# Kernel tuning notes

Hardware: AMD Instinct MI355X
Metric: run time of the kernel (lower is better)

## Reference

```python
import jax, jax.numpy as jnp
import numpy as np

EPS = 1e-5

def setup_inputs() -> dict:
    key = jax.random.key(0)
    ks = jax.random.split(key, 6)
    n, m, k, c_in, c_out = 200000, 50000, 16, 128, 256
    p = jax.random.normal(ks[0], (n, 3), dtype=jnp.float32)
    x = jax.random.normal(ks[1], (n, c_in), dtype=jnp.float32)
    o = jnp.sort(jax.random.randint(ks[2], (4,), 0, n)).astype(jnp.int64)
    n_p = jax.random.normal(ks[3], (m, 3), dtype=jnp.float32)
    knn_idx = jax.random.randint(ks[4], (m, k), 0, n).astype(jnp.int64)
    n_o = jnp.sort(jax.random.randint(ks[5], (4,), 0, m)).astype(jnp.int64)
    norm_w = jnp.ones((c_in,), dtype=jnp.float32)
    norm_b = jnp.zeros((c_in,), dtype=jnp.float32)
    W = jax.random.normal(jax.random.fold_in(key, 7), (c_out, c_in), dtype=jnp.float32) * (1.0 / np.sqrt(c_in))
    return {"p": p, "x": x, "o": o, "n_p": n_p, "knn_idx": knn_idx, "n_o": n_o,
            "norm_w": norm_w, "norm_b": norm_b, "W": W}

def reference(p, x, o, n_p, knn_idx, n_o, norm_w, norm_b, W):
    # Gather neighbor features: [m, k, c_in] (use_xyz=False so grouped_xyz is unused)
    feats = x[knn_idx]
    # LayerNorm over channel dim
    mu = jnp.mean(feats, axis=-1, keepdims=True)
    var = jnp.mean(jnp.square(feats - mu), axis=-1, keepdims=True)
    h = (feats - mu) * jax.lax.rsqrt(var + EPS) * norm_w + norm_b
    # Linear (no bias): torch Linear y = h @ W.T, W: [c_out, c_in]
    y = jnp.einsum('mkc,oc->mko', h, W)
    # MaxPool1d over the k neighbors
    out = jnp.max(y, axis=1)  # [m, c_out]
    return (out, n_p, n_o)
```

## Files before the change

### kernel.cpp

```cpp
#include <hip/hip_runtime.h>


#define C_IN   128
#define C_OUT  256
#define KNN    16
#define LN_EPS 1e-5f
#define BQ     4
#define ROWS   (BQ * KNN)
#define WAVES  8
#define BLOCK  (WAVES * 64)
#define NBLK   1024
#define BROW   128
#define BUFB   (ROWS * BROW)
#define BSCL   16.0f
#define IBSCL  (1.0f / 16.0f)

typedef __attribute__((ext_vector_type(8))) short  short8;
typedef __attribute__((ext_vector_type(4))) short  short4_t;
typedef __attribute__((ext_vector_type(8))) __bf16 bf16x8;
typedef __attribute__((ext_vector_type(4))) float  f32x4;

__device__ __forceinline__ short f2bf_bits(float f) {
    unsigned u = __float_as_uint(f);
    u += 0x7fffu + ((u >> 16) & 1u);
    return (short)(u >> 16);
}

#if defined(__has_builtin) && __has_builtin(__builtin_amdgcn_cvt_pk_fp8_f32)
__device__ __forceinline__ unsigned pk2fp8(float a, float b, unsigned old, bool hi) {
    return hi ? (unsigned)__builtin_amdgcn_cvt_pk_fp8_f32(a, b, (int)old, true)
              : (unsigned)__builtin_amdgcn_cvt_pk_fp8_f32(a, b, (int)old, false);
}
#else
__device__ __forceinline__ unsigned fp8e4m3_byte(float f) {
    unsigned u = __float_as_uint(f);
    const unsigned sgn = (u >> 24) & 0x80u;
    const float af = __uint_as_float(u & 0x7fffffffu);
    if (!(af < 448.f)) return sgn | 0x7Eu;
    if (af < 0.015625f) {
        int q = (int)(af * 512.f + 0.5f);
        return (q > 7) ? (sgn | 0x08u) : (sgn | (unsigned)q);
    }
    unsigned au = u & 0x7fffffffu;
    au += 0x7FFFFu + ((au >> 20) & 1u);
    const int e = (int)(au >> 23) - 127;
    if (e > 8) return sgn | 0x7Eu;
    return sgn | ((unsigned)(e + 7) << 3) | ((au >> 20) & 7u);
}
__device__ __forceinline__ unsigned pk2fp8(float a, float b, unsigned old, bool hi) {
    const unsigned p = fp8e4m3_byte(a) | (fp8e4m3_byte(b) << 8);
    return hi ? ((old & 0xffffu) | (p << 16)) : ((old & 0xffff0000u) | p);
}
#endif

__device__ __forceinline__ void gl_lds16b(const void* src, void* dst) {
    __builtin_amdgcn_global_load_lds(
        (const __attribute__((address_space(1))) void*)src,
        (__attribute__((address_space(3))) void*)dst, 16, 0, 0);
}

__global__ __launch_bounds__(256) void lnq_kernel(
    const float* __restrict__ x, unsigned* __restrict__ xq, int n)
{
    const int r = blockIdx.x * 8 + (threadIdx.x >> 5);
    const int c = threadIdx.x & 31;
    if (r >= n) return;
    const float4 v = *(const float4*)(x + (long long)r * C_IN + c * 4);
    float s1 = v.x + v.y + v.z + v.w;
    float s2 = v.x * v.x + v.y * v.y + v.z * v.z + v.w * v.w;
    #pragma unroll
    for (int off = 1; off < 32; off <<= 1) {
        s1 += __shfl_xor(s1, off);
        s2 += __shfl_xor(s2, off);
    }
    const float mu   = s1 * (1.f / 128.f);
    const float rstd = rsqrtf(s2 * (1.f / 128.f) - mu * mu + LN_EPS);
    unsigned p = pk2fp8((v.x - mu) * rstd, (v.y - mu) * rstd, 0u, false);
    p = pk2fp8((v.z - mu) * rstd, (v.w - mu) * rstd, p, true);
    xq[(long long)r * 32 + c] = p;
}

__global__ __launch_bounds__(BLOCK) void fused_gather_kernel(
    const unsigned char* __restrict__ xq, const int* __restrict__ knn,
    const float* __restrict__ nw, const float* __restrict__ nb,
    const float* __restrict__ W,
    const float* __restrict__ n_p, const int* __restrict__ n_o,
    float* __restrict__ out, float* __restrict__ out_np, float* __restrict__ out_no,
    int mq, int npcnt)
{
    __shared__ __align__(16) char Ash[2 * BUFB];

    const int tid  = threadIdx.x;
    const int lane = tid & 63;
    const int wave = tid >> 6;
    const int m16  = lane & 15;
    const int qd   = lane >> 4;

    const int g    = gridDim.x;
    const int nbat = (mq + BQ - 1) / BQ;
    const int nk   = mq * KNN;

    const int myrow = wave * 8 + (lane >> 3);
    const int sboff = ((lane & 7) ^ (myrow & 7)) * 16;

    int bat = blockIdx.x;
    int i0 = knn[min(bat * ROWS + myrow, nk - 1)];

    long  bfr[2][4];
    float cp0 = 0.f, cp1 = 0.f;
    #pragma unroll
    for (int s = 0; s < 4; ++s) {
        const int k0 = s * 32 + qd * 8;
        const float4 a0 = *(const float4*)(nw + k0);
        const float4 a1 = *(const float4*)(nw + k0 + 4);
        const float4 c0 = *(const float4*)(nb + k0);
        const float4 c1 = *(const float4*)(nb + k0 + 4);
        const float nwv[8] = {a0.x,a0.y,a0.z,a0.w,a1.x,a1.y,a1.z,a1.w};
        const float nbv[8] = {c0.x,c0.y,c0.z,c0.w,c1.x,c1.y,c1.z,c1.w};
        #pragma unroll
        for (int t = 0; t < 2; ++t) {
            const int n_ = wave * 32 + t * 16 + m16;
            const float4* wp = (const float4*)(W + n_ * C_IN + k0);
            const float4 w0 = wp[0], w1 = wp[1];
            const float wvv[8] = {w0.x,w0.y,w0.z,w0.w,w1.x,w1.y,w1.z,w1.w};
            float cacc = 0.f;
            #pragma unroll
            for (int j = 0; j < 8; ++j) cacc += nbv[j] * wvv[j];
            unsigned lo = pk2fp8(wvv[0]*nwv[0]*BSCL, wvv[1]*nwv[1]*BSCL, 0u, false);
            lo = pk2fp8(wvv[2]*nwv[2]*BSCL, wvv[3]*nwv[3]*BSCL, lo, true);
            unsigned hi = pk2fp8(wvv[4]*nwv[4]*BSCL, wvv[5]*nwv[5]*BSCL, 0u, false);
            hi = pk2fp8(wvv[6]*nwv[6]*BSCL, wvv[7]*nwv[7]*BSCL, hi, true);
            bfr[t][s] = (long)(((unsigned long long)hi << 32) | lo);
            if (t == 0) cp0 += cacc; else cp1 += cacc;
        }
    }
    cp0 += __shfl_xor(cp0, 16); cp0 += __shfl_xor(cp0, 32);
    cp1 += __shfl_xor(cp1, 16); cp1 += __shfl_xor(cp1, 32);

    gl_lds16b(xq + (long long)i0 * BROW + sboff, Ash + wave * 1024);
    const int b1 = (bat + g < nbat) ? (bat + g) : bat;
    int inext = knn[min(b1 * ROWS + myrow, nk - 1)];

    int buf = 0;
    for (; bat < nbat; bat += g) {
        __syncthreads();

        if (bat + g < nbat) {
            gl_lds16b(xq + (long long)inext * BROW + sboff,
                      Ash + (buf ^ 1) * BUFB + wave * 1024);
            const int b2 = (bat + 2 * g < nbat) ? (bat + 2 * g) : (bat + g);
            inext = knn[min(b2 * ROWS + myrow, nk - 1)];
        }

        #pragma unroll
        for (int jp = 0; jp < 2; ++jp) {
            float ra0, ra1, rb0, rb1;
            #pragma unroll
            for (int half = 0; half < 2; ++half) {
                const int ql = jp * 2 + half;
                const int r  = ql * 16 + m16;
                long afr[4];
                #pragma unroll
                for (int s = 0; s < 4; ++s) {
                    const int pos = (s * 2 + (qd >> 1)) ^ (r & 7);
                    afr[s] = *(const long*)&Ash[buf * BUFB + r * BROW + pos * 16 + (qd & 1) * 8];
                }
                f32x4 acc0 = {0,0,0,0}, acc1 = {0,0,0,0};
                #pragma unroll
                for (int s = 0; s < 4; ++s) {
                    acc0 = __builtin_amdgcn_mfma_f32_16x16x32_fp8_fp8(
                        afr[s], bfr[0][s], acc0, 0, 0, 0);
                    acc1 = __builtin_amdgcn_mfma_f32_16x16x32_fp8_fp8(
                        afr[s], bfr[1][s], acc1, 0, 0, 0);
                }
                float v0 = fmaxf(fmaxf(acc0[0], acc0[1]), fmaxf(acc0[2], acc0[3]));
                v0 = fmaxf(v0, __shfl_xor(v0, 16));
                v0 = fmaxf(v0, __shfl_xor(v0, 32));
                float v1 = fmaxf(fmaxf(acc1[0], acc1[1]), fmaxf(acc1[2], acc1[3]));
                v1 = fmaxf(v1, __shfl_xor(v1, 16));
                v1 = fmaxf(v1, __shfl_xor(v1, 32));
                if (half == 0) { ra0 = v0; ra1 = v1; }
                else           { rb0 = v0; rb1 = v1; }
            }
            const float s0 = (qd >> 1) ? rb0 : ra0;
            const float s1 = (qd >> 1) ? rb1 : ra1;
            const float val = ((qd & 1) ? s1 : s0) * IBSCL + ((qd & 1) ? cp1 : cp0);
            const int q = bat * BQ + jp * 2 + (qd >> 1);
            if (q < mq)
                out[q * C_OUT + wave * 32 + (qd & 1) * 16 + m16] = val;
        }
        buf ^= 1;
    }

    const int gtid = blockIdx.x * BLOCK + tid;
    const int gstr = g * BLOCK;
    const int np4 = npcnt >> 2;
    for (int i = gtid; i < np4; i += gstr)
        ((float4*)out_np)[i] = ((const float4*)n_p)[i];
    for (int i = (np4 << 2) + gtid; i < npcnt; i += gstr) out_np[i] = n_p[i];
    if (gtid < 4) out_no[gtid] = (float)n_o[gtid];
}

__global__ __launch_bounds__(256) void fused_inline_kernel(
    const float* __restrict__ x, const int* __restrict__ knn,
    const float* __restrict__ nw, const float* __restrict__ nb,
    const float* __restrict__ W,
    const float* __restrict__ n_p, const int* __restrict__ n_o,
    float* __restrict__ out, float* __restrict__ out_np, float* __restrict__ out_no,
    int mq, int npcnt)
{
    __shared__ __align__(16) short Ash[2 * 32 * C_IN];

    const int tid  = threadIdx.x;
    const int lane = tid & 63;
    const int wave = tid >> 6;
    const int m16  = lane & 15;
    const int qd   = lane >> 4;

    short8 bfrag[4][4];
    float  cpart[4] = {0.f, 0.f, 0.f, 0.f};
    #pragma unroll
    for (int s = 0; s < 4; ++s) {
        const int k0 = s * 32 + qd * 8;
        const float4 a0 = *(const float4*)(nw + k0);
        const float4 a1 = *(const float4*)(nw + k0 + 4);
        const float4 c0 = *(const float4*)(nb + k0);
        const float4 c1 = *(const float4*)(nb + k0 + 4);
        const float nwv[8] = {a0.x,a0.y,a0.z,a0.w,a1.x,a1.y,a1.z,a1.w};
        const float nbv[8] = {c0.x,c0.y,c0.z,c0.w,c1.x,c1.y,c1.z,c1.w};
        #pragma unroll
        for (int t = 0; t < 4; ++t) {
            const int n = wave * 64 + t * 16 + m16;
            const float4* wp = (const float4*)(W + n * C_IN + k0);
            const float4 w0 = wp[0], w1 = wp[1];
            const float wvv[8] = {w0.x,w0.y,w0.z,w0.w,w1.x,w1.y,w1.z,w1.w};
            short8 b;
            #pragma unroll
            for (int j = 0; j < 8; ++j) {
                b[j] = f2bf_bits(wvv[j] * nwv[j]);
                cpart[t] += nbv[j] * wvv[j];
            }
            bfrag[t][s] = b;
        }
    }
    #pragma unroll
    for (int t = 0; t < 4; ++t) {
        cpart[t] += __shfl_xor(cpart[t], 16);
        cpart[t] += __shfl_xor(cpart[t], 32);
    }
    const float cbias = (qd == 0) ? cpart[0] : (qd == 1) ? cpart[1]
                      : (qd == 2) ? cpart[2] : cpart[3];

    const int sr = tid >> 3;
    const int sc = tid & 7;

    const int nbat = (mq + 1) / 2;
    const int g = gridDim.x;
    const int nk = mq * KNN;

    int bat = blockIdx.x;
    float4 pf[4];
    int idxn;
    {
        const int id0 = knn[min(bat * 32 + sr, nk - 1)];
        const float* xr = x + (long long)id0 * C_IN + sc * 4;
        #pragma unroll
        for (int t = 0; t < 4; ++t) pf[t] = *(const float4*)(xr + t * 32);
        const int b1 = (bat + g < nbat) ? (bat + g) : bat;
        idxn = knn[min(b1 * 32 + sr, nk - 1)];
    }

    int buf = 0;
    for (; bat < nbat; bat += g) {
        float s1 = 0.f, s2 = 0.f;
        #pragma unroll
        for (int t = 0; t < 4; ++t) {
            s1 += pf[t].x + pf[t].y + pf[t].z + pf[t].w;
            s2 += pf[t].x*pf[t].x + pf[t].y*pf[t].y + pf[t].z*pf[t].z + pf[t].w*pf[t].w;
        }
        #pragma unroll
        for (int off = 1; off < 8; off <<= 1) {
            s1 += __shfl_xor(s1, off);
            s2 += __shfl_xor(s2, off);
        }
        const float mu   = s1 * (1.f / 128.f);
        const float rstd = rsqrtf(s2 * (1.f / 128.f) - mu * mu + LN_EPS);
        #pragma unroll
        for (int t = 0; t < 4; ++t) {
            short4_t hb;
            hb[0] = f2bf_bits((pf[t].x - mu) * rstd);
            hb[1] = f2bf_bits((pf[t].y - mu) * rstd);
            hb[2] = f2bf_bits((pf[t].z - mu) * rstd);
            hb[3] = f2bf_bits((pf[t].w - mu) * rstd);
            const int pb = ((sc >> 1) + 4 * t) ^ (sr & 15);
            *(short4_t*)&Ash[buf * 4096 + sr * 128 + pb * 8 + (sc & 1) * 4] = hb;
        }
        __syncthreads();

        if (bat + g < nbat) {
            const float* xr = x + (long long)idxn * C_IN + sc * 4;
            #pragma unroll
            for (int t = 0; t < 4; ++t) pf[t] = *(const float4*)(xr + t * 32);
            const int b2 = (bat + 2 * g < nbat) ? (bat + 2 * g) : (bat + g);
            idxn = knn[min(b2 * 32 + sr, nk - 1)];
        }

        #pragma unroll
        for (int ql = 0; ql < 2; ++ql) {
            short8 afrag[4];
            #pragma unroll
            for (int s = 0; s < 4; ++s) {
                const int pb = (s * 4 + qd) ^ m16;
                afrag[s] = *(const short8*)&Ash[buf * 4096 + (ql * 16 + m16) * 128 + pb * 8];
            }
            f32x4 acc[4] = {{0,0,0,0},{0,0,0,0},{0,0,0,0},{0,0,0,0}};
            #pragma unroll
            for (int s = 0; s < 4; ++s) {
                const bf16x8 av = __builtin_bit_cast(bf16x8, afrag[s]);
                #pragma unroll
                for (int t = 0; t < 4; ++t)
                    acc[t] = __builtin_amdgcn_mfma_f32_16x16x32_bf16(
                        av, __builtin_bit_cast(bf16x8, bfrag[t][s]), acc[t], 0, 0, 0);
            }
            float r[4];
            #pragma unroll
            for (int t = 0; t < 4; ++t) {
                float v = fmaxf(fmaxf(acc[t][0], acc[t][1]), fmaxf(acc[t][2], acc[t][3]));
                v = fmaxf(v, __shfl_xor(v, 16));
                v = fmaxf(v, __shfl_xor(v, 32));
                r[t] = v;
            }
            const float vout = ((qd == 0) ? r[0] : (qd == 1) ? r[1]
                              : (qd == 2) ? r[2] : r[3]) + cbias;
            const int q = bat * 2 + ql;
            if (q < mq) out[q * C_OUT + wave * 64 + lane] = vout;
        }
        buf ^= 1;
    }

    const int gtid = blockIdx.x * 256 + tid;
    const int gstr = g * 256;
    const int np4 = npcnt >> 2;
    for (int i = gtid; i < np4; i += gstr)
        ((float4*)out_np)[i] = ((const float4*)n_p)[i];
    for (int i = (np4 << 2) + gtid; i < npcnt; i += gstr) out_np[i] = n_p[i];
    if (gtid < 4) out_no[gtid] = (float)n_o[gtid];
}

extern "C" void kernel_launch(void* const* d_in, const int* in_sizes, int n_in,
                              void* d_out, int out_size, void* d_ws, size_t ws_size,
                              hipStream_t stream)
{
    const float* x   = (const float*)d_in[1];
    const float* n_p = (const float*)d_in[3];
    const int*   knn = (const int*)  d_in[4];
    const int*   n_o = (const int*)  d_in[5];
    const float* nw  = (const float*)d_in[6];
    const float* nb  = (const float*)d_in[7];
    const float* W   = (const float*)d_in[8];
    float* out = (float*)d_out;

    const int n     = in_sizes[1] / C_IN;
    const int mq    = in_sizes[4] / KNN;
    const int npcnt = in_sizes[3];
    float* out_np = out + (size_t)mq * C_OUT;
    float* out_no = out_np + npcnt;

    const size_t ws_need = (size_t)n * BROW;
    if (ws_size >= ws_need) {
        unsigned* xq = (unsigned*)d_ws;
        hipLaunchKernelGGL(lnq_kernel, dim3((n + 7) / 8), dim3(256), 0, stream,
                           x, xq, n);
        hipLaunchKernelGGL(fused_gather_kernel, dim3(NBLK), dim3(BLOCK), 0, stream,
                           (const unsigned char*)xq, knn, nw, nb, W, n_p, n_o,
                           out, out_np, out_no, mq, npcnt);
    } else {
        hipLaunchKernelGGL(fused_inline_kernel, dim3(NBLK), dim3(256), 0, stream,
                           x, knn, nw, nb, W, n_p, n_o, out, out_np, out_no, mq, npcnt);
    }
}
```

Baseline: 236.6 us.

## Deepen gather pipeline to four LDS buffers with preloaded neighbor indices

New measurement: 241.5 us. 1.02x slower.

```diff
diff --git a/kernel.cpp b/kernel.cpp
--- a/kernel.cpp
+++ b/kernel.cpp
@@ -12,6 +12,7 @@
 #define NBLK   1024
 #define BROW   128
 #define BUFB   (ROWS * BROW)
+#define NSLOT  16
 #define BSCL   16.0f
 #define IBSCL  (1.0f / 16.0f)
 
@@ -88,7 +89,8 @@
     float* __restrict__ out, float* __restrict__ out_np, float* __restrict__ out_no,
     int mq, int npcnt)
 {
-    __shared__ __align__(16) char Ash[2 * BUFB];
+    __shared__ __align__(16) char Ash[4 * BUFB];
+    __shared__ int idx_lds[NSLOT * ROWS];
 
     const int tid  = threadIdx.x;
     const int lane = tid & 63;
@@ -102,9 +104,13 @@
 
     const int myrow = wave * 8 + (lane >> 3);
     const int sboff = ((lane & 7) ^ (myrow & 7)) * 16;
-
-    int bat = blockIdx.x;
-    int i0 = knn[min(bat * ROWS + myrow, nk - 1)];
+    char* const dwave = Ash + wave * 1024;
+
+    for (int j = tid; j < NSLOT * ROWS; j += BLOCK) {
+        const long long bb = (long long)blockIdx.x + (long long)(j >> 6) * g;
+        const int bidx = (bb < nbat) ? (int)bb : (nbat - 1);
+        idx_lds[j] = knn[min(bidx * ROWS + (j & 63), nk - 1)];
+    }
 
     long  bfr[2][4];
     float cp0 = 0.f, cp1 = 0.f;
@@ -137,20 +143,31 @@
     cp0 += __shfl_xor(cp0, 16); cp0 += __shfl_xor(cp0, 32);
     cp1 += __shfl_xor(cp1, 16); cp1 += __shfl_xor(cp1, 32);
 
-    gl_lds16b(xq + (long long)i0 * BROW + sboff, Ash + wave * 1024);
-    const int b1 = (bat + g < nbat) ? (bat + g) : bat;
-    int inext = knn[min(b1 * ROWS + myrow, nk - 1)];
-
-    int buf = 0;
-    for (; bat < nbat; bat += g) {
-        __syncthreads();
-
-        if (bat + g < nbat) {
-            gl_lds16b(xq + (long long)inext * BROW + sboff,
-                      Ash + (buf ^ 1) * BUFB + wave * 1024);
-            const int b2 = (bat + 2 * g < nbat) ? (bat + 2 * g) : (bat + g);
-            inext = knn[min(b2 * ROWS + myrow, nk - 1)];
-        }
+    __syncthreads();
+
+    {
+        const int i0 = idx_lds[0 * ROWS + myrow];
+        const int i1 = idx_lds[1 * ROWS + myrow];
+        const int i2 = idx_lds[2 * ROWS + myrow];
+        gl_lds16b(xq + (((long long)i0) << 7) + sboff, dwave + 0 * BUFB);
+        gl_lds16b(xq + (((long long)i1) << 7) + sboff, dwave + 1 * BUFB);
+        gl_lds16b(xq + (((long long)i2) << 7) + sboff, dwave + 2 * BUFB);
+    }
+    int nextidx = idx_lds[3 * ROWS + myrow];
+    asm volatile("s_waitcnt vmcnt(2)" ::: "memory");
+    __builtin_amdgcn_s_barrier();
+    __builtin_amdgcn_sched_barrier(0);
+
+    const int L = (nbat - 1 - blockIdx.x) / g + 1;
+    for (int t = 0; t < L; ++t) {
+        const int bat = blockIdx.x + t * g;
+
+        gl_lds16b(xq + (((long long)nextidx) << 7) + sboff,
+                  dwave + ((t + 3) & 3) * BUFB);
+        const int ns = (t + 4 < NSLOT) ? (t + 4) : (NSLOT - 1);
+        nextidx = idx_lds[ns * ROWS + myrow];
+
+        const char* Ab = Ash + (t & 3) * BUFB;
 
         #pragma unroll
         for (int jp = 0; jp < 2; ++jp) {
@@ -163,7 +180,7 @@
                 #pragma unroll
                 for (int s = 0; s < 4; ++s) {
                     const int pos = (s * 2 + (qd >> 1)) ^ (r & 7);
-                    afr[s] = *(const long*)&Ash[buf * BUFB + r * BROW + pos * 16 + (qd & 1) * 8];
+                    afr[s] = *(const long*)(Ab + r * BROW + pos * 16 + (qd & 1) * 8);
                 }
                 f32x4 acc0 = {0,0,0,0}, acc1 = {0,0,0,0};
                 #pragma unroll
@@ -189,7 +206,10 @@
             if (q < mq)
                 out[q * C_OUT + wave * 32 + (qd & 1) * 16 + m16] = val;
         }
-        buf ^= 1;
+
+        asm volatile("s_waitcnt vmcnt(4)" ::: "memory");
+        __builtin_amdgcn_s_barrier();
+        __builtin_amdgcn_sched_barrier(0);
     }
 
     const int gtid = blockIdx.x * BLOCK + tid;
@@ -369,9 +389,12 @@
     const size_t ws_need = (size_t)n * BROW;
     if (ws_size >= ws_need) {
         unsigned* xq = (unsigned*)d_ws;
+        const int nbat = (mq + BQ - 1) / BQ;
+        int grid = (nbat < NBLK) ? nbat : NBLK;
+        while ((nbat + grid - 1) / grid + 3 > NSLOT) grid *= 2;
         hipLaunchKernelGGL(lnq_kernel, dim3((n + 7) / 8), dim3(256), 0, stream,
                            x, xq, n);
-        hipLaunchKernelGGL(fused_gather_kernel, dim3(NBLK), dim3(BLOCK), 0, stream,
+        hipLaunchKernelGGL(fused_gather_kernel, dim3(grid), dim3(BLOCK), 0, stream,
                            (const unsigned char*)xq, knn, nw, nb, W, n_p, n_o,
                            out, out_np, out_no, mq, npcnt);
     } else {
```
